# Kernel optimization log

Measured on AMD Instinct MI355X. Metric: run time of the kernel, lower is better.

The kernel has to match this reference:

```python
import jax, jax.numpy as jnp
import numpy as np

LN_EPS = 1e-6


def setup_inputs() -> dict:
    key = jax.random.key(0)
    ks = jax.random.split(key, 12)
    B, N, D, M, C, K = 8192, 4096, 2048, 1024, 64, 100
    s_in = 1.0 / np.sqrt(D)
    s_mid = 1.0 / np.sqrt(M)
    s_code = 1.0 / np.sqrt(C)
    return {
        "feat": jax.random.normal(ks[0], (B, D), jnp.float32),
        "emb": jax.random.normal(ks[1], (N, D), jnp.float32),
        "W_k": jax.random.normal(ks[2], (D, M), jnp.float32) * s_in,
        "W_v": jax.random.normal(ks[3], (D, M), jnp.float32) * s_in,
        "W_q": jax.random.normal(ks[4], (D, M), jnp.float32) * s_in,
        "W_hash": jax.random.normal(ks[5], (M, C), jnp.float32) * s_mid,
        "b_hash": jnp.zeros((C,), jnp.float32),
        "ln_gamma": jnp.ones((M,), jnp.float32),
        "ln_beta": jnp.zeros((M,), jnp.float32),
        "W_cls": jax.random.normal(ks[6], (C, K), jnp.float32) * s_code,
        "b_cls": jnp.zeros((K,), jnp.float32),
    }


def reference(feat, emb, W_k, W_v, W_q, W_hash, b_hash, ln_gamma, ln_beta, W_cls, b_cls):
    M = W_q.shape[1]
    k = emb @ W_k            # [N, M]
    v = emb @ W_v            # [N, M]
    q = feat @ W_q           # [B, M]
    # scaled dot-product cross-attention over the context set
    scores = (q @ k.T) / jnp.sqrt(jnp.asarray(M, q.dtype))  # [B, N]
    a = jax.nn.softmax(scores, axis=1)
    attended = (a @ v) * jnp.asarray(0.1, q.dtype) + q       # scaled residual
    # layer norm over last axis (eps=1e-6)
    mu = jnp.mean(attended, axis=-1, keepdims=True)
    var = jnp.var(attended, axis=-1, keepdims=True)
    normed = (attended - mu) * jax.lax.rsqrt(var + LN_EPS) * ln_gamma + ln_beta
    fc_hash = normed @ W_hash + b_hash                        # [B, C]
    # binary_activation with eps=0.5: straight-through binarization of sigmoid
    prob = jax.nn.sigmoid(fc_hash)
    hard = (prob > 0.5).astype(prob.dtype)
    code = jax.lax.stop_gradient(hard - prob) + prob
    fc_cls = code @ W_cls + b_cls                             # [B, K]
    return code, prob, fc_cls
```

## Files before the change

kernel.cpp:

```cpp
#include <hip/hip_runtime.h>
#include <math.h>

#define LN_EPS 1e-6

template <int TRANSB>
__global__ __launch_bounds__(256) void gemm128(const float* __restrict__ A,
                                               const float* __restrict__ B,
                                               float* __restrict__ C,
                                               int Mx, int Nx, int Kx) {
  __shared__ float As[16][132];
  __shared__ float Bs[16][132];
  const int tid = threadIdx.x;
  const int bm = blockIdx.y * 128;
  const int bn = blockIdx.x * 128;
  const int ty = tid >> 4;
  const int tx = tid & 15;

  float acc[2][2][4][4] = {};

  for (int k0 = 0; k0 < Kx; k0 += 16) {
#pragma unroll
    for (int it = 0; it < 2; ++it) {
      const int idx = tid + it * 256;
      const int r = idx >> 2;
      const int c4 = (idx & 3) << 2;
      float4 av = *reinterpret_cast<const float4*>(A + (size_t)(bm + r) * Kx + k0 + c4);
      As[c4 + 0][r] = av.x;
      As[c4 + 1][r] = av.y;
      As[c4 + 2][r] = av.z;
      As[c4 + 3][r] = av.w;
    }
    if (TRANSB) {
#pragma unroll
      for (int it = 0; it < 2; ++it) {
        const int idx = tid + it * 256;
        const int r = idx >> 2;
        const int c4 = (idx & 3) << 2;
        float4 bv = *reinterpret_cast<const float4*>(B + (size_t)(bn + r) * Kx + k0 + c4);
        Bs[c4 + 0][r] = bv.x;
        Bs[c4 + 1][r] = bv.y;
        Bs[c4 + 2][r] = bv.z;
        Bs[c4 + 3][r] = bv.w;
      }
    } else {
#pragma unroll
      for (int it = 0; it < 2; ++it) {
        const int idx = tid + it * 256;
        const int kr = idx >> 5;
        const int c4 = (idx & 31) << 2;
        float4 bv = *reinterpret_cast<const float4*>(B + (size_t)(k0 + kr) * Nx + bn + c4);
        *reinterpret_cast<float4*>(&Bs[kr][c4]) = bv;
      }
    }
    __syncthreads();

#pragma unroll
    for (int kk = 0; kk < 16; ++kk) {
      float a0[4], a1[4], b0[4], b1[4];
      *reinterpret_cast<float4*>(a0) = *reinterpret_cast<const float4*>(&As[kk][ty * 4]);
      *reinterpret_cast<float4*>(a1) = *reinterpret_cast<const float4*>(&As[kk][ty * 4 + 64]);
      *reinterpret_cast<float4*>(b0) = *reinterpret_cast<const float4*>(&Bs[kk][tx * 4]);
      *reinterpret_cast<float4*>(b1) = *reinterpret_cast<const float4*>(&Bs[kk][tx * 4 + 64]);
#pragma unroll
      for (int i = 0; i < 4; ++i)
#pragma unroll
        for (int j = 0; j < 4; ++j) {
          acc[0][0][i][j] = fmaf(a0[i], b0[j], acc[0][0][i][j]);
          acc[0][1][i][j] = fmaf(a0[i], b1[j], acc[0][1][i][j]);
          acc[1][0][i][j] = fmaf(a1[i], b0[j], acc[1][0][i][j]);
          acc[1][1][i][j] = fmaf(a1[i], b1[j], acc[1][1][i][j]);
        }
    }
    __syncthreads();
  }

#pragma unroll
  for (int ri = 0; ri < 2; ++ri)
#pragma unroll
    for (int i = 0; i < 4; ++i) {
      const size_t row = (size_t)(bm + ri * 64 + ty * 4 + i);
#pragma unroll
      for (int ci = 0; ci < 2; ++ci) {
        float4 o = make_float4(acc[ri][ci][i][0], acc[ri][ci][i][1], acc[ri][ci][i][2],
                               acc[ri][ci][i][3]);
        *reinterpret_cast<float4*>(C + row * Nx + bn + ci * 64 + tx * 4) = o;
      }
    }
}

__global__ __launch_bounds__(256) void gemm128_kv(const float* __restrict__ A,
                                                  const float* __restrict__ W_k,
                                                  const float* __restrict__ W_v,
                                                  float* __restrict__ kOut,
                                                  float* __restrict__ vOut,
                                                  int Mx, int Nx, int Kx) {
  const float* __restrict__ B = (blockIdx.z == 0) ? W_k : W_v;
  float* __restrict__ C = (blockIdx.z == 0) ? kOut : vOut;

  __shared__ float As[16][132];
  __shared__ float Bs[16][132];
  const int tid = threadIdx.x;
  const int bm = blockIdx.y * 128;
  const int bn = blockIdx.x * 128;
  const int ty = tid >> 4;
  const int tx = tid & 15;

  float acc[2][2][4][4] = {};

  for (int k0 = 0; k0 < Kx; k0 += 16) {
#pragma unroll
    for (int it = 0; it < 2; ++it) {
      const int idx = tid + it * 256;
      const int r = idx >> 2;
      const int c4 = (idx & 3) << 2;
      float4 av = *reinterpret_cast<const float4*>(A + (size_t)(bm + r) * Kx + k0 + c4);
      As[c4 + 0][r] = av.x;
      As[c4 + 1][r] = av.y;
      As[c4 + 2][r] = av.z;
      As[c4 + 3][r] = av.w;
    }
#pragma unroll
    for (int it = 0; it < 2; ++it) {
      const int idx = tid + it * 256;
      const int kr = idx >> 5;
      const int c4 = (idx & 31) << 2;
      float4 bv = *reinterpret_cast<const float4*>(B + (size_t)(k0 + kr) * Nx + bn + c4);
      *reinterpret_cast<float4*>(&Bs[kr][c4]) = bv;
    }
    __syncthreads();

#pragma unroll
    for (int kk = 0; kk < 16; ++kk) {
      float a0[4], a1[4], b0[4], b1[4];
      *reinterpret_cast<float4*>(a0) = *reinterpret_cast<const float4*>(&As[kk][ty * 4]);
      *reinterpret_cast<float4*>(a1) = *reinterpret_cast<const float4*>(&As[kk][ty * 4 + 64]);
      *reinterpret_cast<float4*>(b0) = *reinterpret_cast<const float4*>(&Bs[kk][tx * 4]);
      *reinterpret_cast<float4*>(b1) = *reinterpret_cast<const float4*>(&Bs[kk][tx * 4 + 64]);
#pragma unroll
      for (int i = 0; i < 4; ++i)
#pragma unroll
        for (int j = 0; j < 4; ++j) {
          acc[0][0][i][j] = fmaf(a0[i], b0[j], acc[0][0][i][j]);
          acc[0][1][i][j] = fmaf(a0[i], b1[j], acc[0][1][i][j]);
          acc[1][0][i][j] = fmaf(a1[i], b0[j], acc[1][0][i][j]);
          acc[1][1][i][j] = fmaf(a1[i], b1[j], acc[1][1][i][j]);
        }
    }
    __syncthreads();
  }

#pragma unroll
  for (int ri = 0; ri < 2; ++ri)
#pragma unroll
    for (int i = 0; i < 4; ++i) {
      const size_t row = (size_t)(bm + ri * 64 + ty * 4 + i);
#pragma unroll
      for (int ci = 0; ci < 2; ++ci) {
        float4 o = make_float4(acc[ri][ci][i][0], acc[ri][ci][i][1], acc[ri][ci][i][2],
                               acc[ri][ci][i][3]);
        *reinterpret_cast<float4*>(C + row * Nx + bn + ci * 64 + tx * 4) = o;
      }
    }
}

__global__ __launch_bounds__(256) void softmax_rows(float* __restrict__ S) {
  const size_t row = blockIdx.x;
  float* p = S + row * 4096;
  const int tid = threadIdx.x;
  const int wid = tid >> 6, lane = tid & 63;
  __shared__ float red[4];

  float x[16];
#pragma unroll
  for (int i = 0; i < 4; ++i) {
    float4 v = *reinterpret_cast<const float4*>(p + i * 1024 + tid * 4);
    x[i * 4 + 0] = v.x;
    x[i * 4 + 1] = v.y;
    x[i * 4 + 2] = v.z;
    x[i * 4 + 3] = v.w;
  }
  float m = x[0];
#pragma unroll
  for (int i = 1; i < 16; ++i) m = fmaxf(m, x[i]);
  for (int off = 32; off; off >>= 1) m = fmaxf(m, __shfl_xor(m, off));
  if (lane == 0) red[wid] = m;
  __syncthreads();
  if (tid == 0) red[0] = fmaxf(fmaxf(red[0], red[1]), fmaxf(red[2], red[3]));
  __syncthreads();
  m = red[0];

  const float sc = 0.03125f;
  float e[16];
  float s = 0.f;
#pragma unroll
  for (int i = 0; i < 16; ++i) {
    e[i] = expf((x[i] - m) * sc);
    s += e[i];
  }
  for (int off = 32; off; off >>= 1) s += __shfl_xor(s, off);
  if (lane == 0) red[wid] = s;
  __syncthreads();
  if (tid == 0) red[0] = red[0] + red[1] + red[2] + red[3];
  __syncthreads();
  const float inv = 1.f / red[0];

#pragma unroll
  for (int i = 0; i < 4; ++i) {
    float4 v = make_float4(e[i * 4 + 0] * inv, e[i * 4 + 1] * inv, e[i * 4 + 2] * inv,
                           e[i * 4 + 3] * inv);
    *reinterpret_cast<float4*>(p + i * 1024 + tid * 4) = v;
  }
}

__global__ __launch_bounds__(256) void ln_resid(const float* __restrict__ attRaw,
                                                const float* __restrict__ q,
                                                const float* __restrict__ gamma,
                                                const float* __restrict__ beta,
                                                float* __restrict__ out) {
  const size_t row = blockIdx.x;
  const int tid = threadIdx.x;
  const int wid = tid >> 6, lane = tid & 63;
  __shared__ double redd[4];

  float4 a = *reinterpret_cast<const float4*>(attRaw + row * 1024 + tid * 4);
  float4 qq = *reinterpret_cast<const float4*>(q + row * 1024 + tid * 4);
  float x[4];
  x[0] = fmaf(0.1f, a.x, qq.x);
  x[1] = fmaf(0.1f, a.y, qq.y);
  x[2] = fmaf(0.1f, a.z, qq.z);
  x[3] = fmaf(0.1f, a.w, qq.w);

  double s = (double)x[0] + (double)x[1] + (double)x[2] + (double)x[3];
  for (int off = 32; off; off >>= 1) s += __shfl_xor(s, off);
  if (lane == 0) redd[wid] = s;
  __syncthreads();
  if (tid == 0) redd[0] = redd[0] + redd[1] + redd[2] + redd[3];
  __syncthreads();
  const double mu = redd[0] * (1.0 / 1024.0);
  __syncthreads();

  double d2 = 0.0;
#pragma unroll
  for (int i = 0; i < 4; ++i) {
    double d = (double)x[i] - mu;
    d2 += d * d;
  }
  for (int off = 32; off; off >>= 1) d2 += __shfl_xor(d2, off);
  if (lane == 0) redd[wid] = d2;
  __syncthreads();
  if (tid == 0) redd[0] = redd[0] + redd[1] + redd[2] + redd[3];
  __syncthreads();
  const double var = redd[0] * (1.0 / 1024.0);
  const float rs = (float)(1.0 / sqrt(var + (double)LN_EPS));
  const float muf = (float)mu;

  float4 g = *reinterpret_cast<const float4*>(gamma + tid * 4);
  float4 bb = *reinterpret_cast<const float4*>(beta + tid * 4);
  float4 o;
  o.x = fmaf((x[0] - muf) * rs, g.x, bb.x);
  o.y = fmaf((x[1] - muf) * rs, g.y, bb.y);
  o.z = fmaf((x[2] - muf) * rs, g.z, bb.z);
  o.w = fmaf((x[3] - muf) * rs, g.w, bb.w);
  *reinterpret_cast<float4*>(out + row * 1024 + tid * 4) = o;
}

__global__ __launch_bounds__(128) void head_kernel(const float* __restrict__ normed,
                                                   const float* __restrict__ W_hash,
                                                   const float* __restrict__ b_hash,
                                                   const float* __restrict__ W_cls,
                                                   const float* __restrict__ b_cls,
                                                   float* __restrict__ out_code,
                                                   float* __restrict__ out_prob,
                                                   float* __restrict__ out_cls) {
  __shared__ float ns[1024];
  __shared__ float cs[64];
  const size_t b = blockIdx.x;
  const int tid = threadIdx.x;

#pragma unroll
  for (int i = 0; i < 2; ++i) {
    const int idx = (tid + i * 128) * 4;
    *reinterpret_cast<float4*>(&ns[idx]) =
        *reinterpret_cast<const float4*>(normed + b * 1024 + idx);
  }
  __syncthreads();

  if (tid < 64) {
    double acc = 0.0;
#pragma unroll 4
    for (int m = 0; m < 1024; ++m)
      acc = fma((double)ns[m], (double)W_hash[m * 64 + tid], acc);
    const float fc = (float)(acc + (double)b_hash[tid]);
    const float pr = 1.f / (1.f + expf(-fc));
    const float code = fc > 0.f ? 1.f : 0.f;
    out_code[b * 64 + tid] = code;
    out_prob[b * 64 + tid] = pr;
    cs[tid] = code;
  }
  __syncthreads();

  if (tid < 100) {
    float acc = b_cls[tid];
#pragma unroll 8
    for (int c = 0; c < 64; ++c)
      if (cs[c] != 0.f) acc += W_cls[c * 100 + tid];
    out_cls[b * 100 + tid] = acc;
  }
}

extern "C" void kernel_launch(void* const* d_in, const int* in_sizes, int n_in,
                              void* d_out, int out_size, void* d_ws, size_t ws_size,
                              hipStream_t stream) {
  const float* feat = (const float*)d_in[0];
  const float* emb = (const float*)d_in[1];
  const float* W_k = (const float*)d_in[2];
  const float* W_v = (const float*)d_in[3];
  const float* W_q = (const float*)d_in[4];
  const float* W_hash = (const float*)d_in[5];
  const float* b_hash = (const float*)d_in[6];
  const float* ln_g = (const float*)d_in[7];
  const float* ln_b = (const float*)d_in[8];
  const float* W_cls = (const float*)d_in[9];
  const float* b_cls = (const float*)d_in[10];
  float* out = (float*)d_out;

  const int B = 8192, N = 4096, D = 2048, M = 1024;

  float* ws = (float*)d_ws;
  float* k = ws;
  float* v = k + (size_t)N * M;
  float* q = v + (size_t)N * M;
  float* S = q + (size_t)B * M;

  const size_t fixed = (size_t)2 * N * M + (size_t)2 * B * M;
  const size_t avail = ws_size / sizeof(float);
  int chunk = 8192;
  while (chunk > 128 && fixed + (size_t)chunk * N > avail) chunk >>= 1;
  float* att = S + (size_t)chunk * N;

  gemm128_kv<<<dim3(M / 128, N / 128, 2), 256, 0, stream>>>(emb, W_k, W_v, k, v, N, M, D);
  gemm128<0><<<dim3(M / 128, B / 128), 256, 0, stream>>>(feat, W_q, q, B, M, D);

  for (int c0 = 0; c0 < B; c0 += chunk) {
    const float* qc = q + (size_t)c0 * M;
    gemm128<1><<<dim3(N / 128, chunk / 128), 256, 0, stream>>>(qc, k, S, chunk, N, M);
    softmax_rows<<<chunk, 256, 0, stream>>>(S);
    gemm128<0><<<dim3(M / 128, chunk / 128), 256, 0, stream>>>(S, v, att + (size_t)c0 * M,
                                                               chunk, M, N);
  }

  ln_resid<<<B, 256, 0, stream>>>(att, q, ln_g, ln_b, att);

  head_kernel<<<B, 128, 0, stream>>>(att, W_hash, b_hash, W_cls, b_cls, out,
                                     out + (size_t)B * 64, out + (size_t)B * 128);
}
```

Before: 2.702 ms.

## Run attention GEMMs on bf16x3 split MFMA instead of scalar FP32

Replaces the FP32 SIMT GEMMs for QK^T and PV with an MFMA kernel that splits each FP32 operand into three bf16 parts and sums six cross products, approximating FP32 accuracy on matrix cores. New kernels split q and k, transpose-split v, and softmax now writes the probabilities as three bf16 planes. This adds extra split passes and about three times the memory traffic for the operands, and the workspace layout grows, which may shrink the chunk size.

Measured after the change: 3.698 ms. +36.9%, slower.

```diff
diff --git a/kernel.cpp b/kernel.cpp
--- a/kernel.cpp
+++ b/kernel.cpp
@@ -2,6 +2,25 @@
 #include <math.h>
 
 #define LN_EPS 1e-6
+
+typedef __attribute__((ext_vector_type(8))) short short8v;
+typedef __attribute__((ext_vector_type(4))) float f32x4;
+typedef unsigned short u16;
+
+__device__ __forceinline__ u16 bf16rn(float x) {
+  unsigned int u = __float_as_uint(x);
+  return (u16)((u + 0x7FFFu + ((u >> 16) & 1u)) >> 16);
+}
+__device__ __forceinline__ float bf16tof(u16 h) {
+  return __uint_as_float(((unsigned int)h) << 16);
+}
+__device__ __forceinline__ void split3f(float x, u16& h, u16& m, u16& l) {
+  h = bf16rn(x);
+  float r1 = x - bf16tof(h);
+  m = bf16rn(r1);
+  float r2 = r1 - bf16tof(m);
+  l = bf16rn(r2);
+}
 
 template <int TRANSB>
 __global__ __launch_bounds__(256) void gemm128(const float* __restrict__ A,
@@ -163,9 +182,126 @@
     }
 }
 
-__global__ __launch_bounds__(256) void softmax_rows(float* __restrict__ S) {
+__global__ __launch_bounds__(256, 2) void mfma_bt(
+    const u16* __restrict__ Ah, const u16* __restrict__ Am, const u16* __restrict__ Al,
+    const u16* __restrict__ Bh, const u16* __restrict__ Bm, const u16* __restrict__ Bl,
+    float* __restrict__ C, int Mx, int Nx, int Kx) {
+  __shared__ u16 lds[6 * 128 * 40];
+  const int tid = threadIdx.x;
+  const int lane = tid & 63;
+  const int wid = tid >> 6;
+  const int wr = wid >> 1, wc = wid & 1;
+  const int bm = blockIdx.y * 128, bn = blockIdx.x * 128;
+
+  f32x4 acc[4][4] = {};
+
+  for (int k0 = 0; k0 < Kx; k0 += 32) {
+    const u16* srcs[6] = {Ah, Am, Al, Bh, Bm, Bl};
+#pragma unroll
+    for (int t = 0; t < 6; ++t) {
+      const u16* sp = srcs[t];
+      const int rbase = (t < 3) ? bm : bn;
+#pragma unroll
+      for (int it = 0; it < 2; ++it) {
+        const int gidx = tid + it * 256;
+        const int row = gidx >> 2;
+        const int slot = gidx & 3;
+        uint4 d = *reinterpret_cast<const uint4*>(sp + (size_t)(rbase + row) * Kx + k0 +
+                                                  slot * 8);
+        *reinterpret_cast<uint4*>(&lds[t * 5120 + row * 40 + slot * 8]) = d;
+      }
+    }
+    __syncthreads();
+
+    short8v a[4][3], b[4][3];
+#pragma unroll
+    for (int r = 0; r < 4; ++r)
+#pragma unroll
+      for (int t = 0; t < 3; ++t)
+        a[r][t] = *reinterpret_cast<const short8v*>(
+            &lds[t * 5120 + (wr * 64 + r * 16 + (lane & 15)) * 40 + (lane >> 4) * 8]);
+#pragma unroll
+    for (int c = 0; c < 4; ++c)
+#pragma unroll
+      for (int t = 0; t < 3; ++t)
+        b[c][t] = *reinterpret_cast<const short8v*>(
+            &lds[(3 + t) * 5120 + (wc * 64 + c * 16 + (lane & 15)) * 40 + (lane >> 4) * 8]);
+
+#pragma unroll
+    for (int r = 0; r < 4; ++r)
+#pragma unroll
+      for (int c = 0; c < 4; ++c) {
+        f32x4 t0 = acc[r][c];
+        t0 = __builtin_amdgcn_mfma_f32_16x16x32_bf16(a[r][0], b[c][0], t0, 0, 0, 0);
+        t0 = __builtin_amdgcn_mfma_f32_16x16x32_bf16(a[r][0], b[c][1], t0, 0, 0, 0);
+        t0 = __builtin_amdgcn_mfma_f32_16x16x32_bf16(a[r][1], b[c][0], t0, 0, 0, 0);
+        t0 = __builtin_amdgcn_mfma_f32_16x16x32_bf16(a[r][1], b[c][1], t0, 0, 0, 0);
+        t0 = __builtin_amdgcn_mfma_f32_16x16x32_bf16(a[r][0], b[c][2], t0, 0, 0, 0);
+        t0 = __builtin_amdgcn_mfma_f32_16x16x32_bf16(a[r][2], b[c][0], t0, 0, 0, 0);
+        acc[r][c] = t0;
+      }
+    __syncthreads();
+  }
+
+#pragma unroll
+  for (int r = 0; r < 4; ++r)
+#pragma unroll
+    for (int c = 0; c < 4; ++c)
+#pragma unroll
+      for (int j = 0; j < 4; ++j) {
+        const int row = bm + wr * 64 + r * 16 + (lane >> 4) * 4 + j;
+        const int col = bn + wc * 64 + c * 16 + (lane & 15);
+        C[(size_t)row * Nx + col] = acc[r][c][j];
+      }
+}
+
+__global__ __launch_bounds__(256) void split3k(const float* __restrict__ in,
+                                               u16* __restrict__ h, u16* __restrict__ m,
+                                               u16* __restrict__ l, int n4) {
+  for (size_t i = (size_t)blockIdx.x * 256 + threadIdx.x; i < (size_t)n4;
+       i += (size_t)gridDim.x * 256) {
+    float4 v = reinterpret_cast<const float4*>(in)[i];
+    u16 hh[4], mm[4], ll[4];
+    split3f(v.x, hh[0], mm[0], ll[0]);
+    split3f(v.y, hh[1], mm[1], ll[1]);
+    split3f(v.z, hh[2], mm[2], ll[2]);
+    split3f(v.w, hh[3], mm[3], ll[3]);
+    reinterpret_cast<uint2*>(h)[i] = *reinterpret_cast<const uint2*>(hh);
+    reinterpret_cast<uint2*>(m)[i] = *reinterpret_cast<const uint2*>(mm);
+    reinterpret_cast<uint2*>(l)[i] = *reinterpret_cast<const uint2*>(ll);
+  }
+}
+
+__global__ __launch_bounds__(256) void tsplit3(const float* __restrict__ in,
+                                               u16* __restrict__ th, u16* __restrict__ tm,
+                                               u16* __restrict__ tl, int R, int Cc) {
+  __shared__ float t[32][33];
+  const int tid = threadIdx.x;
+  const int tx = tid & 31, ty = tid >> 5;
+  const int r0 = blockIdx.y * 32, c0 = blockIdx.x * 32;
+#pragma unroll
+  for (int j = 0; j < 4; ++j)
+    t[ty + 8 * j][tx] = in[(size_t)(r0 + ty + 8 * j) * Cc + c0 + tx];
+  __syncthreads();
+#pragma unroll
+  for (int j = 0; j < 4; ++j) {
+    const int cl = ty + 8 * j;
+    float x = t[tx][cl];
+    u16 h, m, l;
+    split3f(x, h, m, l);
+    const size_t o = (size_t)(c0 + cl) * R + r0 + tx;
+    th[o] = h;
+    tm[o] = m;
+    tl[o] = l;
+  }
+}
+
+__global__ __launch_bounds__(256) void softmax_split(const float* __restrict__ S,
+                                                     u16* __restrict__ Ph,
+                                                     u16* __restrict__ Pm,
+                                                     u16* __restrict__ Pl) {
   const size_t row = blockIdx.x;
-  float* p = S + row * 4096;
+  const float* p = S + row * 4096;
   const int tid = threadIdx.x;
   const int wid = tid >> 6, lane = tid & 63;
   __shared__ float red[4];
@@ -206,9 +342,13 @@
 
 #pragma unroll
   for (int i = 0; i < 4; ++i) {
-    float4 v = make_float4(e[i * 4 + 0] * inv, e[i * 4 + 1] * inv, e[i * 4 + 2] * inv,
-                           e[i * 4 + 3] * inv);
-    *reinterpret_cast<float4*>(p + i * 1024 + tid * 4) = v;
+    u16 hh[4], mm[4], ll[4];
+#pragma unroll
+    for (int j = 0; j < 4; ++j) split3f(e[i * 4 + j] * inv, hh[j], mm[j], ll[j]);
+    const size_t o = row * 4096 + i * 1024 + tid * 4;
+    *reinterpret_cast<uint2*>(Ph + o) = *reinterpret_cast<const uint2*>(hh);
+    *reinterpret_cast<uint2*>(Pm + o) = *reinterpret_cast<const uint2*>(mm);
+    *reinterpret_cast<uint2*>(Pl + o) = *reinterpret_cast<const uint2*>(ll);
   }
 }
 
@@ -325,32 +465,50 @@
   float* out = (float*)d_out;
 
   const int B = 8192, N = 4096, D = 2048, M = 1024;
+  const size_t NM = (size_t)N * M;
+  const size_t BM = (size_t)B * M;
 
   float* ws = (float*)d_ws;
-  float* k = ws;
-  float* v = k + (size_t)N * M;
-  float* q = v + (size_t)N * M;
-  float* S = q + (size_t)B * M;
-
-  const size_t fixed = (size_t)2 * N * M + (size_t)2 * B * M;
+  float* kf = ws;
+  float* vf = kf + NM;
+  float* qf = vf + NM;
+  float* att = qf + BM;
+  u16* qh = (u16*)(att + BM);
+  u16* qm = qh + BM;
+  u16* ql = qm + BM;
+  u16* kh = ql + BM;
+  u16* km = kh + NM;
+  u16* kl = km + NM;
+  u16* vth = kl + NM;
+  u16* vtm = vth + NM;
+  u16* vtl = vtm + NM;
+  float* Sf = (float*)(vtl + NM);
+
+  const size_t fixedFl = 2 * NM + 2 * BM + (3 * BM + 6 * NM) / 2;
   const size_t avail = ws_size / sizeof(float);
   int chunk = 8192;
-  while (chunk > 128 && fixed + (size_t)chunk * N > avail) chunk >>= 1;
-  float* att = S + (size_t)chunk * N;
-
-  gemm128_kv<<<dim3(M / 128, N / 128, 2), 256, 0, stream>>>(emb, W_k, W_v, k, v, N, M, D);
-  gemm128<0><<<dim3(M / 128, B / 128), 256, 0, stream>>>(feat, W_q, q, B, M, D);
+  while (chunk > 128 && fixedFl + (size_t)chunk * 10240 > avail) chunk >>= 1;
+  u16* Sh = (u16*)(Sf + (size_t)chunk * 4096);
+  u16* Sm = Sh + (size_t)chunk * 4096;
+  u16* Sl = Sm + (size_t)chunk * 4096;
+
+  gemm128_kv<<<dim3(M / 128, N / 128, 2), 256, 0, stream>>>(emb, W_k, W_v, kf, vf, N, M, D);
+  gemm128<0><<<dim3(M / 128, B / 128), 256, 0, stream>>>(feat, W_q, qf, B, M, D);
+
+  split3k<<<2048, 256, 0, stream>>>(qf, qh, qm, ql, (int)(BM / 4));
+  split3k<<<2048, 256, 0, stream>>>(kf, kh, km, kl, (int)(NM / 4));
+  tsplit3<<<dim3(M / 32, N / 32), 256, 0, stream>>>(vf, vth, vtm, vtl, N, M);
 
   for (int c0 = 0; c0 < B; c0 += chunk) {
-    const float* qc = q + (size_t)c0 * M;
-    gemm128<1><<<dim3(N / 128, chunk / 128), 256, 0, stream>>>(qc, k, S, chunk, N, M);
-    softmax_rows<<<chunk, 256, 0, stream>>>(S);
-    gemm128<0><<<dim3(M / 128, chunk / 128), 256, 0, stream>>>(S, v, att + (size_t)c0 * M,
-                                                               chunk, M, N);
-  }
-
-  ln_resid<<<B, 256, 0, stream>>>(att, q, ln_g, ln_b, att);
-
+    mfma_bt<<<dim3(N / 128, chunk / 128), 256, 0, stream>>>(
+        qh + (size_t)c0 * M, qm + (size_t)c0 * M, ql + (size_t)c0 * M,
+        kh, km, kl, Sf, chunk, N, M);
+    softmax_split<<<chunk, 256, 0, stream>>>(Sf, Sh, Sm, Sl);
+    mfma_bt<<<dim3(M / 128, chunk / 128), 256, 0, stream>>>(
+        Sh, Sm, Sl, vth, vtm, vtl, att + (size_t)c0 * M, chunk, M, N);
+  }
+
+  ln_resid<<<B, 256, 0, stream>>>(att, qf, ln_g, ln_b, att);
   head_kernel<<<B, 128, 0, stream>>>(att, W_hash, b_hash, W_cls, b_cls, out,
                                      out + (size_t)B * 64, out + (size_t)B * 128);
 }
```
